# Kernel optimization log

Hardware: AMD Instinct MI355X
Metric: run time of the kernel (lower is better)

The kernel has to match this reference:

```python
import jax, jax.numpy as jnp
import numpy as np

B, L, D_MODEL = 2, 2048, 512
EXPAND = 2
ED = EXPAND * D_MODEL          # d_inner = 1024
N = 16                          # d_state
D_CONV = 4
DT_RANK = (D_MODEL + N - 1) // N  # 32
D_FF = 1024
EPS = 1e-5


def _mamba_params(key, pre):
    ks = jax.random.split(key, 6)
    s = 0.02
    p = {}
    p[pre + 'in_w'] = jax.random.normal(ks[0], (D_MODEL, 2 * ED), jnp.float32) * s
    p[pre + 'conv_w'] = jax.random.normal(ks[1], (ED, 1, D_CONV), jnp.float32) * s
    p[pre + 'conv_b'] = jnp.zeros((ED,), jnp.float32)
    p[pre + 'xproj_w'] = jax.random.normal(ks[2], (ED, DT_RANK + 2 * N), jnp.float32) * s
    p[pre + 'dt_w'] = jax.random.normal(ks[3], (DT_RANK, ED), jnp.float32) * s
    p[pre + 'dt_b'] = jax.random.normal(ks[4], (ED,), jnp.float32) * s
    # S4D-real init: A_log = log(1..N) per channel
    p[pre + 'A_log'] = jnp.log(jnp.broadcast_to(jnp.arange(1, N + 1, dtype=jnp.float32), (ED, N)))
    p[pre + 'D'] = jnp.ones((ED,), jnp.float32)
    p[pre + 'out_w'] = jax.random.normal(ks[5], (ED, D_MODEL), jnp.float32) * s
    return p


def setup_inputs() -> dict:
    key = jax.random.key(0)
    k_x, k_f, k_b, k_ffn = jax.random.split(key, 4)
    inp = {'x': jax.random.normal(k_x, (B, L, D_MODEL), jnp.float32)}
    inp.update(_mamba_params(k_f, 'f_'))
    inp.update(_mamba_params(k_b, 'b_'))
    inp['norm1_g'] = jnp.ones((D_MODEL,), jnp.float32)
    inp['norm1_b'] = jnp.zeros((D_MODEL,), jnp.float32)
    inp['norm2_g'] = jnp.ones((D_MODEL,), jnp.float32)
    inp['norm2_b'] = jnp.zeros((D_MODEL,), jnp.float32)
    k1, k2 = jax.random.split(k_ffn)
    inp['ffn_w1'] = jax.random.normal(k1, (D_MODEL, D_FF), jnp.float32) * 0.02
    inp['ffn_b1'] = jnp.zeros((D_FF,), jnp.float32)
    inp['ffn_w2'] = jax.random.normal(k2, (D_FF, D_MODEL), jnp.float32) * 0.02
    inp['ffn_b2'] = jnp.zeros((D_MODEL,), jnp.float32)
    return inp


def _selective_scan(x, delta, A, Bm, C, Dp):
    # x, delta: (B,L,ED); A: (ED,N); Bm, C: (B,L,N); Dp: (ED,)
    def step(h, inp):
        x_t, d_t, B_t, C_t = inp  # (B,ED),(B,ED),(B,N),(B,N)
        dA = jnp.exp(d_t[..., None] * A)                      # (B,ED,N)
        dBx = (d_t * x_t)[..., None] * B_t[:, None, :]        # (B,ED,N)
        h = dA * h + dBx
        y = jnp.einsum('ben,bn->be', h, C_t)
        return h, y

    h0 = jnp.zeros((x.shape[0], ED, N), x.dtype)
    xs = (x.transpose(1, 0, 2), delta.transpose(1, 0, 2),
          Bm.transpose(1, 0, 2), C.transpose(1, 0, 2))
    _, ys = jax.lax.scan(step, h0, xs)
    return ys.transpose(1, 0, 2) + x * Dp


def _mamba(x, in_w, conv_w, conv_b, xproj_w, dt_w, dt_b, A_log, Dp, out_w):
    xz = x @ in_w                                  # (B,L,2*ED)
    xs, z = jnp.split(xz, 2, axis=-1)
    # depthwise causal conv over time
    xc = jax.lax.conv_general_dilated(
        xs.transpose(0, 2, 1), conv_w, (1,), [(D_CONV - 1, 0)],
        dimension_numbers=('NCH', 'OIH', 'NCH'), feature_group_count=ED)
    xc = jax.nn.silu(xc.transpose(0, 2, 1) + conv_b)          # (B,L,ED)
    dbl = xc @ xproj_w                                        # (B,L,DT_RANK+2N)
    dt = dbl[..., :DT_RANK]
    Bm = dbl[..., DT_RANK:DT_RANK + N]
    C = dbl[..., DT_RANK + N:]
    delta = jax.nn.softplus(dt @ dt_w + dt_b)                 # (B,L,ED)
    A = -jnp.exp(A_log)
    y = _selective_scan(xc, delta, A, Bm, C, Dp)
    y = y * jax.nn.silu(z)
    return y @ out_w


def _layernorm(h, g, b):
    mu = jnp.mean(h, axis=-1, keepdims=True)
    var = jnp.var(h, axis=-1, keepdims=True)
    return (h - mu) * jax.lax.rsqrt(var + EPS) * g + b


def _ffn(h, w1, b1, w2, b2):
    return jnp.maximum(h @ w1 + b1, 0.0) @ w2 + b2


def reference(x,
              f_in_w, f_conv_w, f_conv_b, f_xproj_w, f_dt_w, f_dt_b, f_A_log, f_D, f_out_w,
              b_in_w, b_conv_w, b_conv_b, b_xproj_w, b_dt_w, b_dt_b, b_A_log, b_D, b_out_w,
              norm1_g, norm1_b, norm2_g, norm2_b,
              ffn_w1, ffn_b1, ffn_w2, ffn_b2):
    mf = _mamba(x, f_in_w, f_conv_w, f_conv_b, f_xproj_w, f_dt_w, f_dt_b, f_A_log, f_D, f_out_w)
    mf = _layernorm(mf, norm1_g, norm1_b)
    out_f = _ffn(mf, ffn_w1, ffn_b1, ffn_w2, ffn_b2) + mf
    # NOTE: original code computes norm2 but then uses the UN-normalized
    # backward output (variable shadowing bug); we replicate that faithfully.
    mb = _mamba(jnp.flip(x, axis=1), b_in_w, b_conv_w, b_conv_b, b_xproj_w,
                b_dt_w, b_dt_b, b_A_log, b_D, b_out_w)
    out_b = _ffn(mb, ffn_w1, ffn_b1, ffn_w2, ffn_b2) + mb
    return out_f + out_b
```

## Files before the change

kernel.cpp:

```cpp
#include <hip/hip_runtime.h>
#include <hip/hip_bf16.h>
#include <math.h>


#define BD 2
#define LD 2048
#define DMODEL 512
#define EDIM 1024
#define NST 16
#define DTR 32
#define DFF 1024
#define MROWS (BD*LD)

typedef __hip_bfloat16 bf16;
typedef __bf16 bf16x8 __attribute__((ext_vector_type(8)));
typedef __bf16 bf16x4 __attribute__((ext_vector_type(4)));
typedef float  f32x4  __attribute__((ext_vector_type(4)));

__device__ __forceinline__ float sig_(float x) { return 1.f / (1.f + __expf(-x)); }

__device__ __forceinline__ void glds16(const void* g, void* l)
{
    __builtin_amdgcn_global_load_lds(
        (const __attribute__((address_space(1))) void*)g,
        (__attribute__((address_space(3))) void*)l, 16, 0, 0);
}

__global__ __launch_bounds__(256)
void prep_k(const float* __restrict__ x, bf16* __restrict__ xbf,
            const float* __restrict__ inw_f, const float* __restrict__ inw_b,
            bf16* __restrict__ inwT,
            const float* __restrict__ outw_f, const float* __restrict__ outw_b,
            bf16* __restrict__ outwT,
            const float* __restrict__ fw1, bf16* __restrict__ fw1T,
            const float* __restrict__ fw2, bf16* __restrict__ fw2T)
{
    const int bid = blockIdx.x, tid = threadIdx.x;
    if (bid < 2048) {
        size_t i = (size_t)bid * 1024 + tid * 4;
        float4 v = *(const float4*)(x + i);
        bf16* o = xbf + i;
        o[0] = __float2bfloat16(v.x); o[1] = __float2bfloat16(v.y);
        o[2] = __float2bfloat16(v.z); o[3] = __float2bfloat16(v.w);
        return;
    }
    const float* W; bf16* WT; int R, C, cx, ry;
    if (bid < 4096) {
        int d = (bid - 2048) >> 10, t = (bid - 2048) & 1023;
        W = d ? inw_b : inw_f; WT = inwT + (size_t)d * 2048 * 512;
        R = 512; C = 2048; cx = t & 63; ry = t >> 6;
    } else if (bid < 5120) {
        int d = (bid - 4096) >> 9, t = (bid - 4096) & 511;
        W = d ? outw_b : outw_f; WT = outwT + (size_t)d * 512 * 1024;
        R = 1024; C = 512; cx = t & 15; ry = t >> 4;
    } else if (bid < 5632) {
        int t = bid - 5120; W = fw1; WT = fw1T; R = 512; C = 1024;
        cx = t & 31; ry = t >> 5;
    } else {
        int t = bid - 5632; W = fw2; WT = fw2T; R = 1024; C = 512;
        cx = t & 15; ry = t >> 4;
    }
    __shared__ float tt[32][33];
    const int c0 = cx * 32, r0 = ry * 32;
    const int col = tid & 31, rr = tid >> 5;
#pragma unroll
    for (int p = 0; p < 4; ++p)
        tt[p * 8 + rr][col] = W[(size_t)(r0 + p * 8 + rr) * C + c0 + col];
    __syncthreads();
#pragma unroll
    for (int p = 0; p < 4; ++p)
        WT[(size_t)(c0 + p * 8 + rr) * R + r0 + col] =
            __float2bfloat16(tt[col][p * 8 + rr]);
}

template<int BN, int MODE, bool FLIPD1, bool CATK>
__global__ __launch_bounds__(256)
void bgemm3_k(const bf16* __restrict__ A, size_t Astr, int lda,
              const bf16* __restrict__ BT, size_t Bstr, int ldb,
              const float* __restrict__ bias,
              bf16* __restrict__ Cb, size_t Cstr, int ldc,
              const bf16* __restrict__ mp, size_t mpStr,
              float* __restrict__ outp, int K)
{
    constexpr int BM = 128;
    constexpr int FRm = 4, FRn = BN / 32;
    constexpr int KH = DFF;
    __shared__ __align__(16) bf16 As[BM][32];
    __shared__ __align__(16) bf16 Bs[BN][32];
    const int tid = threadIdx.x;
    const int dir = blockIdx.z;
    const bool flip = FLIPD1 && (dir == 1);
    const bf16* Ad = A + (CATK ? (size_t)0 : (size_t)dir * Astr);
    const bf16* Bd = BT + (size_t)dir * Bstr;
    const int bm = blockIdx.y * BM, bn = blockIdx.x * BN;
    const int wave = tid >> 6, lane = tid & 63;
    const int wm = (wave >> 1) * 64, wn = (wave & 1) * (BN / 2);
    const int lm = lane & 15, lq = lane >> 4;
    const int lrow = lane >> 2, lcol = (lane & 3) * 8;
    f32x4 acc[FRm][FRn] = {};

    for (int k0 = 0; k0 < K; k0 += 32) {
        const bf16* Ab = Ad;
        int ka = k0;
        if (CATK && k0 >= KH) { Ab = A + Astr; ka = k0 - KH; }
        const int kb = CATK ? (k0 & (KH - 1)) : k0;
#pragma unroll
        for (int c = 0; c < 2; ++c) {
            int row = c * 64 + wave * 16 + lrow;
            int gm = bm + row;
            if (flip) gm = (gm & ~(LD - 1)) + (LD - 1 - (gm & (LD - 1)));
            glds16(Ab + (size_t)gm * lda + ka + lcol,
                   &As[c * 64 + wave * 16][0]);
        }
#pragma unroll
        for (int c = 0; c < BN / 64; ++c) {
            int row = c * 64 + wave * 16 + lrow;
            glds16(Bd + (size_t)(bn + row) * ldb + kb + lcol,
                   &Bs[c * 64 + wave * 16][0]);
        }
        __syncthreads();

        bf16x8 af[FRm], bfr[FRn];
#pragma unroll
        for (int i = 0; i < FRm; ++i)
            af[i] = *(const bf16x8*)&As[wm + 16 * i + lm][lq * 8];
#pragma unroll
        for (int j = 0; j < FRn; ++j)
            bfr[j] = *(const bf16x8*)&Bs[wn + 16 * j + lm][lq * 8];
#pragma unroll
        for (int i = 0; i < FRm; ++i)
#pragma unroll
            for (int j = 0; j < FRn; ++j)
                acc[i][j] = __builtin_amdgcn_mfma_f32_16x16x32_bf16(
                    af[i], bfr[j], acc[i][j], 0, 0, 0);
        __syncthreads();
    }

    bf16* Cd = (MODE == 5) ? nullptr : Cb + (size_t)dir * Cstr;
#pragma unroll
    for (int i = 0; i < FRm; ++i) {
#pragma unroll
        for (int j = 0; j < FRn; ++j) {
            int col = bn + wn + 16 * j + lm;
            float bv = (MODE == 2) ? bias[col]
                     : (MODE == 5) ? 2.f * bias[col] : 0.f;
#pragma unroll
            for (int r = 0; r < 4; ++r) {
                int row = bm + wm + 16 * i + lq * 4 + r;
                float v = acc[i][j][r] + bv;
                size_t idx = (size_t)row * ldc + col;
                if (MODE == 0)      Cd[idx] = __float2bfloat16(v);
                else if (MODE == 2) Cd[idx] = __float2bfloat16(fmaxf(v, 0.f));
                else {
                    float m2 = __bfloat162float(mp[idx])
                             + __bfloat162float(mp[mpStr + idx]);
                    outp[idx] = v + m2;
                }
            }
        }
    }
}

__global__ __launch_bounds__(256)
void zgate_k(const bf16* __restrict__ xbf, const bf16* __restrict__ inwT,
             const bf16* __restrict__ y2t_all, bf16* __restrict__ yrow_all)
{
    __shared__ __align__(16) bf16 As[64][40];
    __shared__ __align__(16) bf16 Bs[128][40];
    __shared__ __bf16 sy[64][130];
    const int tid = threadIdx.x;
    const int dir = blockIdx.z;
    const bf16* Bd = inwT + (size_t)dir * (2048 * 512) + (size_t)1024 * 512;
    const bf16* y2t = y2t_all + (size_t)dir * ((size_t)MROWS * EDIM);
    bf16* yrow = yrow_all + (size_t)dir * ((size_t)MROWS * EDIM);
    const int bm = blockIdx.y * 64, bn = blockIdx.x * 128;
    const int wave = tid >> 6, lane = tid & 63;
    const int wm = (wave >> 1) * 32, wn = (wave & 1) * 64;
    const int lm = lane & 15, lq = lane >> 4;
    f32x4 acc[2][4] = {};

    for (int k0 = 0; k0 < 512; k0 += 32) {
        {
            int row = tid >> 2, col = (tid & 3) * 8;
            int gm = bm + row;
            if (dir == 1) gm = (gm & ~(LD - 1)) + (LD - 1 - (gm & (LD - 1)));
            *(bf16x8*)&As[row][col] =
                *(const bf16x8*)(xbf + (size_t)gm * 512 + k0 + col);
        }
#pragma unroll
        for (int p = 0; p < 2; ++p) {
            int row = p * 64 + (tid >> 2), col = (tid & 3) * 8;
            *(bf16x8*)&Bs[row][col] =
                *(const bf16x8*)(Bd + (size_t)(bn + row) * 512 + k0 + col);
        }
        __syncthreads();
        bf16x8 af[2], bfr[4];
#pragma unroll
        for (int i = 0; i < 2; ++i)
            af[i] = *(const bf16x8*)&As[wm + 16 * i + lm][lq * 8];
#pragma unroll
        for (int j = 0; j < 4; ++j)
            bfr[j] = *(const bf16x8*)&Bs[wn + 16 * j + lm][lq * 8];
#pragma unroll
        for (int i = 0; i < 2; ++i)
#pragma unroll
            for (int j = 0; j < 4; ++j)
                acc[i][j] = __builtin_amdgcn_mfma_f32_16x16x32_bf16(
                    af[i], bfr[j], acc[i][j], 0, 0, 0);
        __syncthreads();
    }

    {
        const int b = bm >> 11, l0 = bm & (LD - 1);
        int e = tid >> 1, lh = (tid & 1) * 32;
        const bf16* yp = y2t + ((size_t)b * EDIM + bn + e) * LD + l0 + lh;
#pragma unroll
        for (int i = 0; i < 4; ++i) {
            bf16x8 v = *(const bf16x8*)(yp + i * 8);
#pragma unroll
            for (int j = 0; j < 8; ++j) sy[lh + i * 8 + j][e] = v[j];
        }
    }
    __syncthreads();
#pragma unroll
    for (int i = 0; i < 2; ++i) {
#pragma unroll
        for (int j = 0; j < 4; ++j) {
            int col = bn + wn + 16 * j + lm;
#pragma unroll
            for (int r = 0; r < 4; ++r) {
                int row = bm + wm + 16 * i + lq * 4 + r;
                float z = acc[i][j][r];
                float g = z * sig_(z);
                float y = (float)sy[(row - bm)][col - bn];
                yrow[(size_t)row * EDIM + col] = __float2bfloat16(g * y);
            }
        }
    }
}

__global__ __launch_bounds__(256)
void conv2_k(const bf16* __restrict__ xs2,
             const float* __restrict__ cw_f, const float* __restrict__ cb_f,
             const float* __restrict__ cw_b, const float* __restrict__ cb_b,
             bf16* __restrict__ xct2)
{
    __shared__ float sxs[67][65];
    __shared__ float sout[64][65];
    const int tid = threadIdx.x;
    const int dir = blockIdx.z;
    const bf16* xs = xs2 + (size_t)dir * ((size_t)MROWS * EDIM);
    const float* w  = dir ? cw_b : cw_f;
    const float* cb = dir ? cb_b : cb_f;
    bf16* xct = xct2 + (size_t)dir * ((size_t)MROWS * EDIM);
    const int e0 = blockIdx.x * 64;
    const int bl0 = blockIdx.y * 64;
    const int lloc0 = bl0 & (LD - 1);
    const int b = bl0 >> 11;
    {
        int c8 = (tid & 7) * 8;
#pragma unroll
        for (int i = 0; i < 3; ++i) {
            int hr = i * 32 + (tid >> 3);
            if (hr < 67) {
                int lr = lloc0 + hr - 3;
                if (lr >= 0) {
                    bf16x8 v = *(const bf16x8*)(xs +
                        (size_t)(bl0 + hr - 3) * EDIM + e0 + c8);
#pragma unroll
                    for (int j = 0; j < 8; ++j) sxs[hr][c8 + j] = (float)v[j];
                } else {
#pragma unroll
                    for (int j = 0; j < 8; ++j) sxs[hr][c8 + j] = 0.f;
                }
            }
        }
    }
    __syncthreads();
    {
        int lr4 = tid >> 6, e = tid & 63;
        float w0 = w[(e0 + e) * 4 + 0], w1 = w[(e0 + e) * 4 + 1];
        float w2 = w[(e0 + e) * 4 + 2], w3 = w[(e0 + e) * 4 + 3];
        float cbv = cb[e0 + e];
#pragma unroll
        for (int i = 0; i < 16; ++i) {
            int lr = i * 4 + lr4;
            float acc = cbv;
            acc = fmaf(sxs[lr + 0][e], w0, acc);
            acc = fmaf(sxs[lr + 1][e], w1, acc);
            acc = fmaf(sxs[lr + 2][e], w2, acc);
            acc = fmaf(sxs[lr + 3][e], w3, acc);
            sout[e][lr] = acc * sig_(acc);
        }
    }
    __syncthreads();
    {
        int l8 = (tid & 7) * 8;
#pragma unroll
        for (int i = 0; i < 2; ++i) {
            int er = i * 32 + (tid >> 3);
            bf16x8 o;
#pragma unroll
            for (int j = 0; j < 8; ++j) o[j] = (__bf16)sout[er][l8 + j];
            *(bf16x8*)(xct + ((size_t)b * EDIM + e0 + er) * LD + lloc0 + l8) = o;
        }
    }
}

__global__ __launch_bounds__(256)
void g2_k(const bf16* __restrict__ xct2, const float* __restrict__ xp_f,
          const float* __restrict__ xp_b, float* __restrict__ dblt2)
{
    __shared__ __align__(16) float As[32][18];
    __shared__ __align__(16) float Bs[32][66];
    const int tid = threadIdx.x;
    const int dir = blockIdx.y;
    const bf16* xct = xct2 + (size_t)dir * ((size_t)MROWS * EDIM);
    const float* xproj = dir ? xp_b : xp_f;
    float* dblt = dblt2 + (size_t)dir * (2 * 64 * LD);
    const int r0 = blockIdx.x * 16;
    const int bB = r0 >> 11, l0 = r0 & (LD - 1);
    const int row = tid >> 4, col4 = (tid & 15) * 4;
    float acc[4] = {};

    for (int k0 = 0; k0 < EDIM; k0 += 32) {
        if (tid < 128) {
            int k = tid & 31, ls = (tid >> 5) * 4;
            const bf16* p = xct + ((size_t)bB * EDIM + k0 + k) * LD + l0 + ls;
            bf16x4 v = *(const bf16x4*)p;
            As[k][ls]     = (float)v[0];
            As[k][ls + 1] = (float)v[1];
            As[k][ls + 2] = (float)v[2];
            As[k][ls + 3] = (float)v[3];
        }
        {
            int k = tid >> 3, ns = (tid & 7) * 8;
            const float* p = xproj + (size_t)(k0 + k) * 64 + ns;
            float4 v0 = *(const float4*)p, v1 = *(const float4*)(p + 4);
            float* d = &Bs[k][ns];
            d[0]=v0.x; d[1]=v0.y; d[2]=v0.z; d[3]=v0.w;
            d[4]=v1.x; d[5]=v1.y; d[6]=v1.z; d[7]=v1.w;
        }
        __syncthreads();
#pragma unroll
        for (int kk = 0; kk < 32; ++kk) {
            float a = As[kk][row];
            float4 b4 = *(const float4*)&Bs[kk][col4];
            acc[0] = fmaf(a, b4.x, acc[0]);
            acc[1] = fmaf(a, b4.y, acc[1]);
            acc[2] = fmaf(a, b4.z, acc[2]);
            acc[3] = fmaf(a, b4.w, acc[3]);
        }
        __syncthreads();
    }
#pragma unroll
    for (int j = 0; j < 4; ++j)
        dblt[((size_t)bB * 64 + col4 + j) * LD + l0 + row] = acc[j];
}

__global__ __launch_bounds__(256)
void g3_k(const float* __restrict__ dblt2,
          const float* __restrict__ dtw_f, const float* __restrict__ dtb_f,
          const float* __restrict__ dtw_b, const float* __restrict__ dtb_b,
          bf16* __restrict__ dltt2)
{
    __shared__ __align__(16) float As[16][68];
    __shared__ __align__(16) float Bs[16][68];
    const int tid = threadIdx.x;
    const int dir = blockIdx.z;
    const float* Ap = dblt2 + (size_t)dir * (2 * 64 * LD);
    const float* Bw = dir ? dtw_b : dtw_f;
    const float* bias = dir ? dtb_b : dtb_f;
    bf16* Ct = dltt2 + (size_t)dir * ((size_t)MROWS * EDIM);
    const int bm = blockIdx.y * 64;
    const int bn = blockIdx.x * 64;
    const int bB = bm >> 11, l0 = bm & (LD - 1);
    const int tx = tid & 15, ty = tid >> 4;
    float acc[4][4] = {};

    for (int k0 = 0; k0 < DTR; k0 += 16) {
#pragma unroll
        for (int i = 0; i < 4; ++i) {
            int k = i * 4 + (tid >> 6), ll = tid & 63;
            As[k][ll] = Ap[((size_t)bB * 64 + k0 + k) * LD + l0 + ll];
        }
#pragma unroll
        for (int i = 0; i < 4; ++i) {
            int idx = tid + 256 * i;
            int nl = idx & 63, kl = idx >> 6;
            Bs[kl][nl] = Bw[(size_t)(k0 + kl) * EDIM + bn + nl];
        }
        __syncthreads();
#pragma unroll
        for (int kk = 0; kk < 16; ++kk) {
            float4 av = *(const float4*)&As[kk][ty * 4];
            float4 bv = *(const float4*)&Bs[kk][tx * 4];
            float a[4] = {av.x, av.y, av.z, av.w};
            float b[4] = {bv.x, bv.y, bv.z, bv.w};
#pragma unroll
            for (int i = 0; i < 4; ++i)
#pragma unroll
                for (int j = 0; j < 4; ++j)
                    acc[i][j] = fmaf(a[i], b[j], acc[i][j]);
        }
        __syncthreads();
    }
#pragma unroll
    for (int i = 0; i < 4; ++i) {
        int r = bm + ty * 4 + i;
#pragma unroll
        for (int j = 0; j < 4; ++j) {
            int c = bn + tx * 4 + j;
            float v = acc[i][j] + bias[c];
            v = (v > 20.f) ? v : log1pf(__expf(v));
            Ct[((size_t)(r >> 11) * EDIM + c) * LD + (r & (LD - 1))] =
                __float2bfloat16(v);
        }
    }
}

__global__ __launch_bounds__(256)
void scan6_k(bf16* __restrict__ xct2, const bf16* __restrict__ dltt2,
             const float* __restrict__ dblt2,
             const float* __restrict__ alog_f, const float* __restrict__ alog_b,
             const float* __restrict__ dp_f, const float* __restrict__ dp_b)
{
    __shared__ float sA[NST];
    __shared__ float sWp[NST][4];
    __shared__ float sWs[NST][4];
    const int gid = blockIdx.x;
    const int dir = gid >> 11;
    const int bb  = (gid >> 10) & 1;
    const int e   = gid & (EDIM - 1);
    const float* A_log = dir ? alog_b : alog_f;
    const float* Dp    = dir ? dp_b   : dp_f;
    bf16* xct = xct2 + (size_t)dir * ((size_t)MROWS * EDIM);
    const bf16* dltt = dltt2 + (size_t)dir * ((size_t)MROWS * EDIM);
    const float* bt = dblt2 + (size_t)dir * (2 * 64 * LD) + (size_t)bb * 64 * LD;
    const int tid = threadIdx.x;
    const int wave = tid >> 6, lane = tid & 63;
    const size_t baset = ((size_t)bb * EDIM + e) * LD;
    const int l0 = tid * 8;

    if (tid < NST) sA[tid] = -__expf(A_log[e * NST + tid]);

    float xv[8], dv[8], dx[8];
    {
        bf16x8 xr = *(const bf16x8*)(xct + baset + l0);
        bf16x8 dr = *(const bf16x8*)(dltt + baset + l0);
#pragma unroll
        for (int j = 0; j < 8; ++j) { xv[j] = (float)xr[j]; dv[j] = (float)dr[j]; }
    }
#pragma unroll
    for (int j = 0; j < 8; ++j) dx[j] = dv[j] * xv[j];
    __syncthreads();

    float y[8] = {};
    for (int n = 0; n < NST; ++n) {
        const float An = sA[n];
        const float* Bp = bt + (size_t)(DTR + n) * LD + l0;
        const float* Cp = bt + (size_t)(DTR + NST + n) * LD + l0;
        float4 b0 = *(const float4*)Bp, b1 = *(const float4*)(Bp + 4);
        float4 c0 = *(const float4*)Cp, c1 = *(const float4*)(Cp + 4);
        float Br[8] = {b0.x,b0.y,b0.z,b0.w, b1.x,b1.y,b1.z,b1.w};
        float Cr[8] = {c0.x,c0.y,c0.z,c0.w, c1.x,c1.y,c1.z,c1.w};

        float S[8], P[8];
        float h = 0.f, pr = 1.f;
#pragma unroll
        for (int l = 0; l < 8; ++l) {
            float a = __expf(dv[l] * An);
            pr *= a;
            h = fmaf(a, h, dx[l] * Br[l]);
            P[l] = pr; S[l] = h;
        }

        float p = pr, s = h;
#pragma unroll
        for (int d = 1; d < 64; d <<= 1) {
            float pp = __shfl_up(p, d, 64);
            float sp = __shfl_up(s, d, 64);
            if (lane >= d) { s = fmaf(sp, p, s); p *= pp; }
        }
        if (lane == 63) { sWp[n][wave] = p; sWs[n][wave] = s; }
        __syncthreads();
        float Hoff = 0.f;
#pragma unroll
        for (int w = 0; w < 3; ++w)
            if (w < wave) Hoff = fmaf(sWp[n][w], Hoff, sWs[n][w]);
        float pprev = __shfl_up(p, 1, 64);
        float sprev = __shfl_up(s, 1, 64);
        float H = (lane == 0) ? Hoff : fmaf(pprev, Hoff, sprev);

#pragma unroll
        for (int l = 0; l < 8; ++l)
            y[l] = fmaf(Cr[l], fmaf(P[l], H, S[l]), y[l]);
    }

    const float Dv = Dp[e];
    bf16x8 o;
#pragma unroll
    for (int l = 0; l < 8; ++l) o[l] = (__bf16)fmaf(xv[l], Dv, y[l]);
    *(bf16x8*)(xct + baset + l0) = o;
}

__global__ __launch_bounds__(256)
void ln_k(bf16* __restrict__ m, const float* __restrict__ gg,
          const float* __restrict__ bb)
{
    int row = (blockIdx.x * 256 + threadIdx.x) >> 6;
    int lane = threadIdx.x & 63;
    bf16* r = m + (size_t)row * DMODEL;
    float v[8], s = 0.f, s2 = 0.f;
#pragma unroll
    for (int i = 0; i < 8; ++i) {
        v[i] = __bfloat162float(r[lane + 64 * i]);
        s += v[i]; s2 = fmaf(v[i], v[i], s2);
    }
#pragma unroll
    for (int off = 32; off >= 1; off >>= 1) {
        s  += __shfl_xor(s, off, 64);
        s2 += __shfl_xor(s2, off, 64);
    }
    float mu = s * (1.f / DMODEL);
    float var = s2 * (1.f / DMODEL) - mu * mu;
    float inv = rsqrtf(var + 1e-5f);
#pragma unroll
    for (int i = 0; i < 8; ++i)
        r[lane + 64 * i] = __float2bfloat16(
            (v[i] - mu) * inv * gg[lane + 64 * i] + bb[lane + 64 * i]);
}

__global__ void sentinel_k(float* __restrict__ o)
{
    int i = blockIdx.x * 256 + threadIdx.x;
    o[i] = 100.0f;
}

extern "C" void kernel_launch(void* const* d_in, const int* in_sizes, int n_in,
                              void* d_out, int out_size, void* d_ws, size_t ws_size,
                              hipStream_t stream)
{
    const float* x    = (const float*)d_in[0];
    const float* n1g  = (const float*)d_in[19];
    const float* n1b  = (const float*)d_in[20];
    const float* fw1  = (const float*)d_in[23];
    const float* fb1  = (const float*)d_in[24];
    const float* fw2  = (const float*)d_in[25];
    const float* fb2  = (const float*)d_in[26];
    float* out = (float*)d_out;

    const size_t MiB = 1024 * 1024;
    const size_t SZ_DM = (size_t)MROWS * DMODEL;
    if (ws_size < 46 * MiB) {
        sentinel_k<<<dim3(SZ_DM / 256), dim3(256), 0, stream>>>(out);
        return;
    }

    char* base = (char*)d_ws;
    bf16* fw1T  = (bf16*)base;
    bf16* fw2T  = (bf16*)(base + 1 * MiB);
    bf16* outwT = (bf16*)(base + 2 * MiB);
    bf16* inwT  = (bf16*)(base + 4 * MiB);
    bf16* xbf   = (bf16*)(base + 8 * MiB);
    char* RA    = base + 12 * MiB;
    bf16* xs2   = (bf16*)RA;
    bf16* dltt2 = (bf16*)RA;
    bf16* yrow2 = (bf16*)RA;
    bf16* ffh2  = (bf16*)RA;
    char* RB    = base + 28 * MiB;
    bf16* xct2  = (bf16*)RB;
    bf16* mbf2  = (bf16*)RB;
    float* dblt2 = (float*)(base + 44 * MiB);

    const float* inw_f  = (const float*)d_in[1];
    const float* cw_f   = (const float*)d_in[2];
    const float* cb_f   = (const float*)d_in[3];
    const float* xp_f   = (const float*)d_in[4];
    const float* dtw_f  = (const float*)d_in[5];
    const float* dtb_f  = (const float*)d_in[6];
    const float* alog_f = (const float*)d_in[7];
    const float* dp_f   = (const float*)d_in[8];
    const float* outw_f = (const float*)d_in[9];
    const float* inw_b  = (const float*)d_in[10];
    const float* cw_b   = (const float*)d_in[11];
    const float* cb_b   = (const float*)d_in[12];
    const float* xp_b   = (const float*)d_in[13];
    const float* dtw_b  = (const float*)d_in[14];
    const float* dtb_b  = (const float*)d_in[15];
    const float* alog_b = (const float*)d_in[16];
    const float* dp_b   = (const float*)d_in[17];
    const float* outw_b = (const float*)d_in[18];

    dim3 blk(256);
    const size_t U = (size_t)MROWS * EDIM;

    prep_k<<<dim3(6144), blk, 0, stream>>>(x, xbf, inw_f, inw_b, inwT,
                                           outw_f, outw_b, outwT,
                                           fw1, fw1T, fw2, fw2T);
    bgemm3_k<128, 0, true, false><<<dim3(8, 32, 2), blk, 0, stream>>>(
        xbf, 0, DMODEL, inwT, (size_t)2048 * 512, DMODEL, nullptr,
        xs2, U, EDIM, nullptr, 0, nullptr, DMODEL);
    conv2_k<<<dim3(16, 64, 2), blk, 0, stream>>>(xs2, cw_f, cb_f, cw_b, cb_b, xct2);
    g2_k<<<dim3(256, 2), blk, 0, stream>>>(xct2, xp_f, xp_b, dblt2);
    g3_k<<<dim3(16, 64, 2), blk, 0, stream>>>(dblt2, dtw_f, dtb_f, dtw_b, dtb_b, dltt2);
    scan6_k<<<dim3(4096), blk, 0, stream>>>(xct2, dltt2, dblt2,
                                            alog_f, alog_b, dp_f, dp_b);
    zgate_k<<<dim3(8, 64, 2), blk, 0, stream>>>(xbf, inwT, xct2, yrow2);
    bgemm3_k<64, 0, false, false><<<dim3(8, 32, 2), blk, 0, stream>>>(
        yrow2, U, EDIM, outwT, (size_t)512 * 1024, EDIM, nullptr,
        mbf2, SZ_DM, DMODEL, nullptr, 0, nullptr, EDIM);
    ln_k<<<dim3(MROWS / 4), blk, 0, stream>>>(mbf2, n1g, n1b);
    bgemm3_k<128, 2, false, false><<<dim3(8, 32, 2), blk, 0, stream>>>(
        mbf2, SZ_DM, DMODEL, fw1T, 0, DMODEL, fb1,
        ffh2, U, DFF, nullptr, 0, nullptr, DMODEL);
    bgemm3_k<64, 5, false, true><<<dim3(8, 32, 1), blk, 0, stream>>>(
        ffh2, U, DFF, fw2T, 0, DFF, fb2,
        nullptr, 0, DMODEL, mbf2, SZ_DM, out, 2 * DFF);
}
```

Measured before the change: 423.4 us.

## Move x_proj and dt_proj small GEMMs onto bf16 MFMA with pre-transposed weights

Replaces the scalar-FMA g2/g3 kernels with MFMA-based versions that use bf16 weights transposed in the prep kernel. The x_proj output is split: dt-rank columns go to a row-major buffer for the dt GEMM, and B/C columns go to the transposed layout the scan reads. The aim is to cut the FMA-bound time of these projections. The cost is extra bf16 rounding of activations and weights, a larger workspace, and g2m launching only 128 blocks, which risks low occupancy.

Result: faster. 372.2 us (-12.1%).

```diff
diff --git a/kernel.cpp b/kernel.cpp
--- a/kernel.cpp
+++ b/kernel.cpp
@@ -33,7 +33,11 @@
             const float* __restrict__ outw_f, const float* __restrict__ outw_b,
             bf16* __restrict__ outwT,
             const float* __restrict__ fw1, bf16* __restrict__ fw1T,
-            const float* __restrict__ fw2, bf16* __restrict__ fw2T)
+            const float* __restrict__ fw2, bf16* __restrict__ fw2T,
+            const float* __restrict__ xp_f, const float* __restrict__ xp_b,
+            bf16* __restrict__ xpT,
+            const float* __restrict__ dtw_f, const float* __restrict__ dtw_b,
+            bf16* __restrict__ dtwT)
 {
     const int bid = blockIdx.x, tid = threadIdx.x;
     if (bid < 2048) {
@@ -56,9 +60,17 @@
     } else if (bid < 5632) {
         int t = bid - 5120; W = fw1; WT = fw1T; R = 512; C = 1024;
         cx = t & 31; ry = t >> 5;
-    } else {
+    } else if (bid < 6144) {
         int t = bid - 5632; W = fw2; WT = fw2T; R = 1024; C = 512;
         cx = t & 15; ry = t >> 4;
+    } else if (bid < 6272) {
+        int d = (bid - 6144) >> 6, t = (bid - 6144) & 63;
+        W = d ? xp_b : xp_f; WT = xpT + (size_t)d * 64 * 1024;
+        R = 1024; C = 64; cx = t & 1; ry = t >> 1;
+    } else {
+        int d = (bid - 6272) >> 5, t = (bid - 6272) & 31;
+        W = d ? dtw_b : dtw_f; WT = dtwT + (size_t)d * 1024 * DTR;
+        R = 32; C = 1024; cx = t; ry = 0;
     }
     __shared__ float tt[32][33];
     const int c0 = cx * 32, r0 = ry * 32;
@@ -308,113 +320,160 @@
 }
 
 __global__ __launch_bounds__(256)
-void g2_k(const bf16* __restrict__ xct2, const float* __restrict__ xp_f,
-          const float* __restrict__ xp_b, float* __restrict__ dblt2)
-{
-    __shared__ __align__(16) float As[32][18];
-    __shared__ __align__(16) float Bs[32][66];
-    const int tid = threadIdx.x;
-    const int dir = blockIdx.y;
-    const bf16* xct = xct2 + (size_t)dir * ((size_t)MROWS * EDIM);
-    const float* xproj = dir ? xp_b : xp_f;
-    float* dblt = dblt2 + (size_t)dir * (2 * 64 * LD);
-    const int r0 = blockIdx.x * 16;
-    const int bB = r0 >> 11, l0 = r0 & (LD - 1);
-    const int row = tid >> 4, col4 = (tid & 15) * 4;
-    float acc[4] = {};
-
-    for (int k0 = 0; k0 < EDIM; k0 += 32) {
-        if (tid < 128) {
-            int k = tid & 31, ls = (tid >> 5) * 4;
-            const bf16* p = xct + ((size_t)bB * EDIM + k0 + k) * LD + l0 + ls;
-            bf16x4 v = *(const bf16x4*)p;
-            As[k][ls]     = (float)v[0];
-            As[k][ls + 1] = (float)v[1];
-            As[k][ls + 2] = (float)v[2];
-            As[k][ls + 3] = (float)v[3];
-        }
-        {
-            int k = tid >> 3, ns = (tid & 7) * 8;
-            const float* p = xproj + (size_t)(k0 + k) * 64 + ns;
-            float4 v0 = *(const float4*)p, v1 = *(const float4*)(p + 4);
-            float* d = &Bs[k][ns];
-            d[0]=v0.x; d[1]=v0.y; d[2]=v0.z; d[3]=v0.w;
-            d[4]=v1.x; d[5]=v1.y; d[6]=v1.z; d[7]=v1.w;
-        }
-        __syncthreads();
-#pragma unroll
-        for (int kk = 0; kk < 32; ++kk) {
-            float a = As[kk][row];
-            float4 b4 = *(const float4*)&Bs[kk][col4];
-            acc[0] = fmaf(a, b4.x, acc[0]);
-            acc[1] = fmaf(a, b4.y, acc[1]);
-            acc[2] = fmaf(a, b4.z, acc[2]);
-            acc[3] = fmaf(a, b4.w, acc[3]);
-        }
-        __syncthreads();
-    }
-#pragma unroll
-    for (int j = 0; j < 4; ++j)
-        dblt[((size_t)bB * 64 + col4 + j) * LD + l0 + row] = acc[j];
-}
-
-__global__ __launch_bounds__(256)
-void g3_k(const float* __restrict__ dblt2,
-          const float* __restrict__ dtw_f, const float* __restrict__ dtb_f,
-          const float* __restrict__ dtw_b, const float* __restrict__ dtb_b,
-          bf16* __restrict__ dltt2)
-{
-    __shared__ __align__(16) float As[16][68];
-    __shared__ __align__(16) float Bs[16][68];
+void g2m_k(const bf16* __restrict__ xct2, const bf16* __restrict__ xpT2,
+           float* __restrict__ dblt2, float* __restrict__ dbldt2)
+{
+    __shared__ float As[64][33];
+    __shared__ __align__(16) bf16 Bs[64][32];
+    __shared__ float sC[32][65];
     const int tid = threadIdx.x;
     const int dir = blockIdx.z;
-    const float* Ap = dblt2 + (size_t)dir * (2 * 64 * LD);
-    const float* Bw = dir ? dtw_b : dtw_f;
+    const bf16* xct = xct2 + (size_t)dir * ((size_t)MROWS * EDIM);
+    const bf16* xpT = xpT2 + (size_t)dir * (64 * 1024);
+    float* dblt = dblt2 + (size_t)dir * (2 * 64 * LD);
+    float* dbldt = dbldt2 + (size_t)dir * (2 * 2048 * DTR);
+    const int bm = blockIdx.y * 64;
+    const int bB = bm >> 11, l0 = bm & (LD - 1);
+    const int wave = tid >> 6, lane = tid & 63;
+    const int wm = (wave >> 1) * 32, wn = (wave & 1) * 32;
+    const int lm = lane & 15, lq = lane >> 4;
+    const int er = tid >> 3, l8 = (tid & 7) * 8;
+    f32x4 acc[2][2] = {};
+
+    for (int k0 = 0; k0 < EDIM; k0 += 32) {
+        glds16(xpT + (size_t)(wave * 16 + (lane >> 2)) * 1024 + k0 + (lane & 3) * 8,
+               &Bs[wave * 16][0]);
+        {
+            bf16x8 v = *(const bf16x8*)(xct +
+                ((size_t)bB * EDIM + k0 + er) * LD + l0 + l8);
+#pragma unroll
+            for (int j = 0; j < 8; ++j) As[l8 + j][er] = (float)v[j];
+        }
+        __syncthreads();
+        bf16x8 af[2], bfr[2];
+#pragma unroll
+        for (int i = 0; i < 2; ++i) {
+            int row = wm + 16 * i + lm;
+#pragma unroll
+            for (int j = 0; j < 8; ++j) af[i][j] = (__bf16)As[row][lq * 8 + j];
+        }
+#pragma unroll
+        for (int j = 0; j < 2; ++j)
+            bfr[j] = *(const bf16x8*)&Bs[wn + 16 * j + lm][lq * 8];
+#pragma unroll
+        for (int i = 0; i < 2; ++i)
+#pragma unroll
+            for (int j = 0; j < 2; ++j)
+                acc[i][j] = __builtin_amdgcn_mfma_f32_16x16x32_bf16(
+                    af[i], bfr[j], acc[i][j], 0, 0, 0);
+        __syncthreads();
+    }
+    if (wn == 0) {
+#pragma unroll
+        for (int i = 0; i < 2; ++i)
+#pragma unroll
+            for (int j = 0; j < 2; ++j) {
+                int col = 16 * j + lm;
+#pragma unroll
+                for (int r = 0; r < 4; ++r) {
+                    int row = wm + 16 * i + lq * 4 + r;
+                    dbldt[(size_t)(bB * 2048 + l0 + row) * DTR + col] =
+                        acc[i][j][r];
+                }
+            }
+    } else {
+#pragma unroll
+        for (int i = 0; i < 2; ++i)
+#pragma unroll
+            for (int j = 0; j < 2; ++j) {
+                int col = 16 * j + lm;
+#pragma unroll
+                for (int r = 0; r < 4; ++r)
+                    sC[col][wm + 16 * i + lq * 4 + r] = acc[i][j][r];
+            }
+    }
+    __syncthreads();
+    {
+        int nr = tid >> 3, ll = (tid & 7) * 8;
+        float4 v0 = *(const float4*)&sC[nr][ll];
+        float4 v1 = *(const float4*)&sC[nr][ll + 4];
+        float* d = dblt + (size_t)(bB * 64 + 32 + nr) * LD + l0 + ll;
+        *(float4*)d = v0; *(float4*)(d + 4) = v1;
+    }
+}
+
+__global__ __launch_bounds__(256)
+void g3m_k(const float* __restrict__ dbldt2, const bf16* __restrict__ dtwT2,
+           const float* __restrict__ dtb_f, const float* __restrict__ dtb_b,
+           bf16* __restrict__ dltt2)
+{
+    __shared__ __align__(16) bf16 As[64][40];
+    __shared__ __align__(16) bf16 Bs[64][32];
+    __shared__ float sC[64][65];
+    const int tid = threadIdx.x;
+    const int dir = blockIdx.z;
+    const float* Ap = dbldt2 + (size_t)dir * (2 * 2048 * DTR);
+    const bf16* BT = dtwT2 + (size_t)dir * (1024 * DTR);
     const float* bias = dir ? dtb_b : dtb_f;
-    bf16* Ct = dltt2 + (size_t)dir * ((size_t)MROWS * EDIM);
-    const int bm = blockIdx.y * 64;
-    const int bn = blockIdx.x * 64;
+    bf16* dltt = dltt2 + (size_t)dir * ((size_t)MROWS * EDIM);
+    const int bm = blockIdx.y * 64, bn = blockIdx.x * 64;
     const int bB = bm >> 11, l0 = bm & (LD - 1);
-    const int tx = tid & 15, ty = tid >> 4;
-    float acc[4][4] = {};
-
-    for (int k0 = 0; k0 < DTR; k0 += 16) {
-#pragma unroll
-        for (int i = 0; i < 4; ++i) {
-            int k = i * 4 + (tid >> 6), ll = tid & 63;
-            As[k][ll] = Ap[((size_t)bB * 64 + k0 + k) * LD + l0 + ll];
-        }
-#pragma unroll
-        for (int i = 0; i < 4; ++i) {
-            int idx = tid + 256 * i;
-            int nl = idx & 63, kl = idx >> 6;
-            Bs[kl][nl] = Bw[(size_t)(k0 + kl) * EDIM + bn + nl];
-        }
-        __syncthreads();
-#pragma unroll
-        for (int kk = 0; kk < 16; ++kk) {
-            float4 av = *(const float4*)&As[kk][ty * 4];
-            float4 bv = *(const float4*)&Bs[kk][tx * 4];
-            float a[4] = {av.x, av.y, av.z, av.w};
-            float b[4] = {bv.x, bv.y, bv.z, bv.w};
-#pragma unroll
-            for (int i = 0; i < 4; ++i)
-#pragma unroll
-                for (int j = 0; j < 4; ++j)
-                    acc[i][j] = fmaf(a[i], b[j], acc[i][j]);
-        }
-        __syncthreads();
-    }
-#pragma unroll
-    for (int i = 0; i < 4; ++i) {
-        int r = bm + ty * 4 + i;
-#pragma unroll
-        for (int j = 0; j < 4; ++j) {
-            int c = bn + tx * 4 + j;
-            float v = acc[i][j] + bias[c];
-            v = (v > 20.f) ? v : log1pf(__expf(v));
-            Ct[((size_t)(r >> 11) * EDIM + c) * LD + (r & (LD - 1))] =
-                __float2bfloat16(v);
+    const int wave = tid >> 6, lane = tid & 63;
+    const int wm = (wave >> 1) * 32, wn = (wave & 1) * 32;
+    const int lm = lane & 15, lq = lane >> 4;
+
+    {
+        int row = tid >> 2, c8 = (tid & 3) * 8;
+        const float* p = Ap + (size_t)(bB * 2048 + l0 + row) * DTR + c8;
+        float4 v0 = *(const float4*)p, v1 = *(const float4*)(p + 4);
+        bf16x8 o;
+        o[0]=(__bf16)v0.x; o[1]=(__bf16)v0.y; o[2]=(__bf16)v0.z; o[3]=(__bf16)v0.w;
+        o[4]=(__bf16)v1.x; o[5]=(__bf16)v1.y; o[6]=(__bf16)v1.z; o[7]=(__bf16)v1.w;
+        *(bf16x8*)&As[row][c8] = o;
+    }
+    glds16(BT + (size_t)(bn + wave * 16 + (lane >> 2)) * DTR + (lane & 3) * 8,
+           &Bs[wave * 16][0]);
+    __syncthreads();
+
+    bf16x8 af[2], bfr[2];
+#pragma unroll
+    for (int i = 0; i < 2; ++i)
+        af[i] = *(const bf16x8*)&As[wm + 16 * i + lm][lq * 8];
+#pragma unroll
+    for (int j = 0; j < 2; ++j)
+        bfr[j] = *(const bf16x8*)&Bs[wn + 16 * j + lm][lq * 8];
+    f32x4 acc[2][2] = {};
+#pragma unroll
+    for (int i = 0; i < 2; ++i)
+#pragma unroll
+        for (int j = 0; j < 2; ++j)
+            acc[i][j] = __builtin_amdgcn_mfma_f32_16x16x32_bf16(
+                af[i], bfr[j], acc[i][j], 0, 0, 0);
+
+#pragma unroll
+    for (int i = 0; i < 2; ++i)
+#pragma unroll
+        for (int j = 0; j < 2; ++j) {
+            int col = wn + 16 * j + lm;
+            float bv = bias[bn + col];
+#pragma unroll
+            for (int r = 0; r < 4; ++r) {
+                int row = wm + 16 * i + lq * 4 + r;
+                float v = acc[i][j][r] + bv;
+                v = (v > 20.f) ? v : log1pf(__expf(v));
+                sC[col][row] = v;
+            }
+        }
+    __syncthreads();
+    {
+        int erow = tid >> 2, l16 = (tid & 3) * 16;
+        bf16* d = dltt + ((size_t)bB * EDIM + bn + erow) * LD + l0 + l16;
+#pragma unroll
+        for (int h = 0; h < 2; ++h) {
+            bf16x8 o;
+#pragma unroll
+            for (int j = 0; j < 8; ++j) o[j] = (__bf16)sC[erow][l16 + h * 8 + j];
+            *(bf16x8*)(d + h * 8) = o;
         }
     }
 }
@@ -552,7 +611,7 @@
 
     const size_t MiB = 1024 * 1024;
     const size_t SZ_DM = (size_t)MROWS * DMODEL;
-    if (ws_size < 46 * MiB) {
+    if (ws_size < 49 * MiB) {
         sentinel_k<<<dim3(SZ_DM / 256), dim3(256), 0, stream>>>(out);
         return;
     }
@@ -572,6 +631,9 @@
     bf16* xct2  = (bf16*)RB;
     bf16* mbf2  = (bf16*)RB;
     float* dblt2 = (float*)(base + 44 * MiB);
+    float* dbldt2 = (float*)(base + 46 * MiB);
+    bf16* xpT2  = (bf16*)(base + 48 * MiB);
+    bf16* dtwT2 = (bf16*)(base + 48 * MiB + 256 * 1024);
 
     const float* inw_f  = (const float*)d_in[1];
     const float* cw_f   = (const float*)d_in[2];
@@ -595,15 +657,17 @@
     dim3 blk(256);
     const size_t U = (size_t)MROWS * EDIM;
 
-    prep_k<<<dim3(6144), blk, 0, stream>>>(x, xbf, inw_f, inw_b, inwT,
+    prep_k<<<dim3(6336), blk, 0, stream>>>(x, xbf, inw_f, inw_b, inwT,
                                            outw_f, outw_b, outwT,
-                                           fw1, fw1T, fw2, fw2T);
+                                           fw1, fw1T, fw2, fw2T,
+                                           xp_f, xp_b, xpT2,
+                                           dtw_f, dtw_b, dtwT2);
     bgemm3_k<128, 0, true, false><<<dim3(8, 32, 2), blk, 0, stream>>>(
         xbf, 0, DMODEL, inwT, (size_t)2048 * 512, DMODEL, nullptr,
         xs2, U, EDIM, nullptr, 0, nullptr, DMODEL);
     conv2_k<<<dim3(16, 64, 2), blk, 0, stream>>>(xs2, cw_f, cb_f, cw_b, cb_b, xct2);
-    g2_k<<<dim3(256, 2), blk, 0, stream>>>(xct2, xp_f, xp_b, dblt2);
-    g3_k<<<dim3(16, 64, 2), blk, 0, stream>>>(dblt2, dtw_f, dtb_f, dtw_b, dtb_b, dltt2);
+    g2m_k<<<dim3(1, 64, 2), blk, 0, stream>>>(xct2, xpT2, dblt2, dbldt2);
+    g3m_k<<<dim3(16, 64, 2), blk, 0, stream>>>(dbldt2, dtwT2, dtb_f, dtb_b, dltt2);
     scan6_k<<<dim3(4096), blk, 0, stream>>>(xct2, dltt2, dblt2,
                                             alog_f, alog_b, dp_f, dp_b);
     zgate_k<<<dim3(8, 64, 2), blk, 0, stream>>>(xbf, inwT, xct2, yrow2);
```
